# Kernel optimization log

Hardware: AMD Instinct MI355X
Metric: run time of the kernel (lower is better)

Reference implementation:

```python
import jax, jax.numpy as jnp
import numpy as np

MAX_DISP = 40
STRIDE_2 = 1
EPS = 1e-06  # hardcoded in the torch module's CosineSimilarity


def setup_inputs() -> dict:
    key = jax.random.key(0)
    k1, k2 = jax.random.split(key)
    B, C, H, W = 4, 256, 128, 256
    x_1 = jax.random.normal(k1, (B, C, H, W), dtype=jnp.float32)
    x_2 = jax.random.normal(k2, (B, C, H, W), dtype=jnp.float32)
    return {"x_1": x_1, "x_2": x_2}


def reference(x_1, x_2):
    B, C, H, W = x_1.shape
    # pad x_2 on the right of the width axis by max_disp (zeros)
    x2p = jnp.pad(x_2, ((0, 0), (0, 0), (0, 0), (0, MAX_DISP)))
    # channel L2 norms computed ONCE (the fusion opportunity)
    n1 = jnp.sqrt(jnp.sum(x_1 * x_1, axis=1))            # [B, H, W]
    n2p = jnp.sqrt(jnp.sum(x2p * x2p, axis=1))           # [B, H, W+D]
    sims = []
    for d in range(0, MAX_DISP + 1, STRIDE_2):           # fixed small set of 41 shifts
        x2s = jax.lax.dynamic_slice_in_dim(x2p, d, W, axis=3)   # [B, C, H, W]
        n2 = jax.lax.dynamic_slice_in_dim(n2p, d, W, axis=2)    # [B, H, W]
        dot = jnp.einsum('bchw,bchw->bhw', x_1, x2s)
        sims.append(dot / jnp.maximum(n1 * n2, EPS))
    return jnp.stack(sims, axis=1)                       # [B, 41, H, W]
```

## Files before the change

kernel.cpp:

```cpp
#include <hip/hip_runtime.h>
#include <hip/hip_bf16.h>


#define B_   4
#define C_   256
#define H_   128
#define W_   256
#define ND_  41
#define HW_  (H_ * W_)
#define CHW_ (C_ * HW_)
#define EPS_ 1e-6f

typedef __attribute__((ext_vector_type(4))) float f32x4;
typedef __attribute__((ext_vector_type(8))) short bf16x8;

#define ABASE 0
#define BBASE 20480
#define NBASE 44800
#define LDSZ  47040

#define PHASE_BAR() do {                                         \
    __builtin_amdgcn_sched_barrier(0);                           \
    asm volatile("s_waitcnt lgkmcnt(0)" ::: "memory");           \
    __builtin_amdgcn_s_barrier();                                \
    __builtin_amdgcn_sched_barrier(0);                           \
  } while (0)

__device__ __forceinline__ unsigned bfr(float x) {
  unsigned u = __builtin_bit_cast(unsigned, x);
  return (u + 0x7fffu + ((u >> 16) & 1u)) >> 16;
}

__global__ __launch_bounds__(512, 4)
void corr_mfma(const float* __restrict__ x1, const float* __restrict__ x2,
               float* __restrict__ out) {
  __shared__ __align__(16) char lds[LDSZ];

  const int tid = threadIdx.x;
  const int l   = tid & 63;
  const int v   = tid >> 6;
  const int m   = l & 15;
  const int g   = l >> 4;

  const int r = blockIdx.x;
  const int b = r >> 7;
  const int h = r & (H_ - 1);

  const float* X1 = x1 + b * CHW_ + h * W_;
  const float* X2 = x2 + b * CHW_ + h * W_;

  if (tid < 560) ((float*)(lds + NBASE))[tid] = 0.f;
  {
    unsigned* zp = (unsigned*)(lds + BBASE + 256 * 80);
    zp[tid] = 0u;
    if (tid < 960 - 512) zp[tid + 512] = 0u;
  }

  int wadr1[4];
#pragma unroll
  for (int j = 0; j < 4; ++j) {
    int w = 4 * l + j;
    wadr1[j] = ABASE + w * 80 + (((v >> 1) + w) % 5) * 16 + (v & 1) * 8;
  }
  int adrA[2], adrB[2][4];
#pragma unroll
  for (int i = 0; i < 2; ++i) {
    int wt = v + 8 * i;
    int rowA = 16 * wt + m;
    adrA[i] = ABASE + rowA * 80 + ((g + rowA) % 5) * 16;
#pragma unroll
    for (int c = 0; c < 4; ++c) {
      int col = 16 * (wt + c) + m;
      adrB[i][c] = BBASE + col * 80 + ((g + col) % 5) * 16;
    }
  }

  f32x4 acc[2][4];
#pragma unroll
  for (int i = 0; i < 2; ++i)
#pragma unroll
    for (int c = 0; c < 4; ++c) acc[i][c] = (f32x4){0.f, 0.f, 0.f, 0.f};
  float ssq1[4] = {0.f, 0.f, 0.f, 0.f}, ssq2[4] = {0.f, 0.f, 0.f, 0.f};

  f32x4 r1[4], r2[4];
  auto loadset = [&](int ks) {
    const float* p1 = X1 + (ks * 32 + 4 * v) * HW_ + 4 * l;
    const float* p2 = X2 + (ks * 32 + 4 * v) * HW_ + 4 * l;
#pragma unroll
    for (int i = 0; i < 4; ++i) {
      r1[i] = *(const f32x4*)(p1 + i * HW_);
      r2[i] = *(const f32x4*)(p2 + i * HW_);
    }
  };

  loadset(0);

  for (int ks = 0; ks < 8; ++ks) {
    PHASE_BAR();
#pragma unroll
    for (int j = 0; j < 4; ++j) {
#pragma unroll
      for (int i = 0; i < 4; ++i) {
        ssq1[j] += r1[i][j] * r1[i][j];
        ssq2[j] += r2[i][j] * r2[i][j];
      }
      uint2 p1, p2;
      p1.x = bfr(r1[0][j]) | (bfr(r1[1][j]) << 16);
      p1.y = bfr(r1[2][j]) | (bfr(r1[3][j]) << 16);
      p2.x = bfr(r2[0][j]) | (bfr(r2[1][j]) << 16);
      p2.y = bfr(r2[2][j]) | (bfr(r2[3][j]) << 16);
      *(uint2*)(lds + wadr1[j]) = p1;
      *(uint2*)(lds + wadr1[j] + (BBASE - ABASE)) = p2;
    }
    if (ks < 7) loadset(ks + 1);
    PHASE_BAR();
    bf16x8 a0 = *(const bf16x8*)(lds + adrA[0]);
    bf16x8 a1 = *(const bf16x8*)(lds + adrA[1]);
#pragma unroll
    for (int c = 0; c < 4; ++c) {
      bf16x8 b0 = *(const bf16x8*)(lds + adrB[0][c]);
      acc[0][c] = __builtin_amdgcn_mfma_f32_16x16x32_bf16(a0, b0, acc[0][c], 0, 0, 0);
    }
#pragma unroll
    for (int c = 0; c < 4; ++c) {
      bf16x8 b1 = *(const bf16x8*)(lds + adrB[1][c]);
      acc[1][c] = __builtin_amdgcn_mfma_f32_16x16x32_bf16(a1, b1, acc[1][c], 0, 0, 0);
    }
  }

  float* nsq = (float*)(lds + NBASE);
#pragma unroll
  for (int j = 0; j < 4; ++j) {
    atomicAdd(nsq + 4 * l + j, ssq1[j]);
    atomicAdd(nsq + 256 + 4 * l + j, ssq2[j]);
  }
  __syncthreads();
  if (tid < 512) nsq[tid] = sqrtf(nsq[tid]);
  if (tid < 48)  nsq[512 + tid] = sqrtf(nsq[512 + tid]);
  __syncthreads();

  float* Sw  = (float*)(lds + v * 4224);
  float* n1s = nsq;
  float* n2s = nsq + 256;
  const int wq = l & 3, dd = l >> 2;
#pragma unroll
  for (int i = 0; i < 2; ++i) {
    int wt = v + 8 * i;
#pragma unroll
    for (int c = 0; c < 4; ++c)
#pragma unroll
      for (int rr = 0; rr < 4; ++rr)
        Sw[(4 * g + rr) * 66 + 16 * c + m] = acc[i][c][rr];
#pragma unroll
    for (int p = 0; p < 3; ++p) {
      int d  = 16 * p + dd;
      int w0 = 16 * wt + 4 * wq;
      f32x4 o;
#pragma unroll
      for (int j = 0; j < 4; ++j) {
        int mm = 4 * wq + j;
        float dot = Sw[mm * 66 + mm + d];
        o[j] = dot / fmaxf(n1s[w0 + j] * n2s[w0 + j + d], EPS_);
      }
      if (d <= 40)
        *(f32x4*)(out + ((b * ND_ + d) * H_ + h) * W_ + w0) = o;
    }
  }
}

extern "C" void kernel_launch(void* const* d_in, const int* in_sizes, int n_in,
                              void* d_out, int out_size, void* d_ws, size_t ws_size,
                              hipStream_t stream) {
  const float* x1 = (const float*)d_in[0];
  const float* x2 = (const float*)d_in[1];
  float* out = (float*)d_out;
  dim3 grid(B_ * H_);
  dim3 block(512);
  hipLaunchKernelGGL(corr_mfma, grid, block, 0, stream, x1, x2, out);
}
```

Measured before the change: 58.19 us.

## Double-buffer global loads two K-steps ahead with named register sets

Replaces the single register staging set with two alternating sets (A/B) and fully unrolls the eight K-steps, so global loads are issued two iterations ahead instead of one. This aims to hide more HBM latency behind the pack and MFMA phases. It doubles the staging registers (32 extra VGPRs), which may hurt occupancy under the 512x4 launch bound or cause spills.

```diff
diff --git a/kernel.cpp b/kernel.cpp
--- a/kernel.cpp
+++ b/kernel.cpp
@@ -82,51 +82,65 @@
     for (int c = 0; c < 4; ++c) acc[i][c] = (f32x4){0.f, 0.f, 0.f, 0.f};
   float ssq1[4] = {0.f, 0.f, 0.f, 0.f}, ssq2[4] = {0.f, 0.f, 0.f, 0.f};
 
-  f32x4 r1[4], r2[4];
-  auto loadset = [&](int ks) {
-    const float* p1 = X1 + (ks * 32 + 4 * v) * HW_ + 4 * l;
-    const float* p2 = X2 + (ks * 32 + 4 * v) * HW_ + 4 * l;
-#pragma unroll
-    for (int i = 0; i < 4; ++i) {
-      r1[i] = *(const f32x4*)(p1 + i * HW_);
-      r2[i] = *(const f32x4*)(p2 + i * HW_);
-    }
-  };
+  f32x4 r1A0, r1A1, r1A2, r1A3, r2A0, r2A1, r2A2, r2A3;
+  f32x4 r1B0, r1B1, r1B2, r1B3, r2B0, r2B1, r2B2, r2B3;
 
-  loadset(0);
+#define LOADSET(S, ks_) do {                                         \
+    const float* _p1 = X1 + ((ks_) * 32 + 4 * v) * HW_ + 4 * l;      \
+    const float* _p2 = X2 + ((ks_) * 32 + 4 * v) * HW_ + 4 * l;      \
+    r1##S##0 = *(const f32x4*)(_p1);           r2##S##0 = *(const f32x4*)(_p2);           \
+    r1##S##1 = *(const f32x4*)(_p1 + HW_);     r2##S##1 = *(const f32x4*)(_p2 + HW_);     \
+    r1##S##2 = *(const f32x4*)(_p1 + 2 * HW_); r2##S##2 = *(const f32x4*)(_p2 + 2 * HW_); \
+    r1##S##3 = *(const f32x4*)(_p1 + 3 * HW_); r2##S##3 = *(const f32x4*)(_p2 + 3 * HW_); \
+  } while (0)
 
-  for (int ks = 0; ks < 8; ++ks) {
-    PHASE_BAR();
-#pragma unroll
-    for (int j = 0; j < 4; ++j) {
-#pragma unroll
-      for (int i = 0; i < 4; ++i) {
-        ssq1[j] += r1[i][j] * r1[i][j];
-        ssq2[j] += r2[i][j] * r2[i][j];
-      }
-      uint2 p1, p2;
-      p1.x = bfr(r1[0][j]) | (bfr(r1[1][j]) << 16);
-      p1.y = bfr(r1[2][j]) | (bfr(r1[3][j]) << 16);
-      p2.x = bfr(r2[0][j]) | (bfr(r2[1][j]) << 16);
-      p2.y = bfr(r2[2][j]) | (bfr(r2[3][j]) << 16);
-      *(uint2*)(lds + wadr1[j]) = p1;
-      *(uint2*)(lds + wadr1[j] + (BBASE - ABASE)) = p2;
-    }
-    if (ks < 7) loadset(ks + 1);
-    PHASE_BAR();
-    bf16x8 a0 = *(const bf16x8*)(lds + adrA[0]);
-    bf16x8 a1 = *(const bf16x8*)(lds + adrA[1]);
-#pragma unroll
-    for (int c = 0; c < 4; ++c) {
-      bf16x8 b0 = *(const bf16x8*)(lds + adrB[0][c]);
-      acc[0][c] = __builtin_amdgcn_mfma_f32_16x16x32_bf16(a0, b0, acc[0][c], 0, 0, 0);
-    }
-#pragma unroll
-    for (int c = 0; c < 4; ++c) {
-      bf16x8 b1 = *(const bf16x8*)(lds + adrB[1][c]);
-      acc[1][c] = __builtin_amdgcn_mfma_f32_16x16x32_bf16(a1, b1, acc[1][c], 0, 0, 0);
-    }
-  }
+#define PACK(S) do {                                                          \
+    _Pragma("unroll")                                                         \
+    for (int j = 0; j < 4; ++j) {                                             \
+      ssq1[j] += r1##S##0[j] * r1##S##0[j] + r1##S##1[j] * r1##S##1[j]        \
+               + r1##S##2[j] * r1##S##2[j] + r1##S##3[j] * r1##S##3[j];       \
+      ssq2[j] += r2##S##0[j] * r2##S##0[j] + r2##S##1[j] * r2##S##1[j]        \
+               + r2##S##2[j] * r2##S##2[j] + r2##S##3[j] * r2##S##3[j];       \
+      uint2 q1, q2;                                                           \
+      q1.x = bfr(r1##S##0[j]) | (bfr(r1##S##1[j]) << 16);                     \
+      q1.y = bfr(r1##S##2[j]) | (bfr(r1##S##3[j]) << 16);                     \
+      q2.x = bfr(r2##S##0[j]) | (bfr(r2##S##1[j]) << 16);                     \
+      q2.y = bfr(r2##S##2[j]) | (bfr(r2##S##3[j]) << 16);                     \
+      *(uint2*)(lds + wadr1[j]) = q1;                                         \
+      *(uint2*)(lds + wadr1[j] + BBASE) = q2;                                 \
+    }                                                                         \
+  } while (0)
+
+#define MFMA_STEP() do {                                                      \
+    bf16x8 a0 = *(const bf16x8*)(lds + adrA[0]);                              \
+    bf16x8 a1 = *(const bf16x8*)(lds + adrA[1]);                              \
+    _Pragma("unroll")                                                         \
+    for (int c = 0; c < 4; ++c) {                                             \
+      bf16x8 b0 = *(const bf16x8*)(lds + adrB[0][c]);                         \
+      acc[0][c] = __builtin_amdgcn_mfma_f32_16x16x32_bf16(a0, b0, acc[0][c], 0, 0, 0); \
+    }                                                                         \
+    _Pragma("unroll")                                                         \
+    for (int c = 0; c < 4; ++c) {                                             \
+      bf16x8 b1 = *(const bf16x8*)(lds + adrB[1][c]);                         \
+      acc[1][c] = __builtin_amdgcn_mfma_f32_16x16x32_bf16(a1, b1, acc[1][c], 0, 0, 0); \
+    }                                                                         \
+  } while (0)
+
+#define BODY(S, ks_) do {                                                     \
+    PHASE_BAR();                              \
+    PACK(S);                                 \
+    if ((ks_) < 6) LOADSET(S, (ks_) + 2);       \
+    PHASE_BAR();                                          \
+    MFMA_STEP();                                                              \
+  } while (0)
+
+  LOADSET(A, 0);
+  LOADSET(B, 1);
+
+  BODY(A, 0); BODY(B, 1);
+  BODY(A, 2); BODY(B, 3);
+  BODY(A, 4); BODY(B, 5);
+  BODY(A, 6); BODY(B, 7);
 
   float* nsq = (float*)(lds + NBASE);
 #pragma unroll
```

Measured after the change: 97.45 us. +67.5%, slower.

## Split each row across two blocks with an x2 halo for finer-grained work

Applied to the files above, without the earlier changes.

Each block now handles half a row (128 columns) with 256 threads instead of a full row with 512 threads, which doubles the grid. The first half loads an extra 40-column halo of x2; the second half writes zeros for the padding instead. Shared memory per block drops by about half, so more blocks can fit per CU and work spreads more evenly across CUs. The cost is redundant halo reads of x2 and extra per-block setup and norm reduction.

```diff
diff --git a/kernel.cpp b/kernel.cpp
--- a/kernel.cpp
+++ b/kernel.cpp
@@ -15,9 +15,9 @@
 typedef __attribute__((ext_vector_type(8))) short bf16x8;
 
 #define ABASE 0
-#define BBASE 20480
-#define NBASE 44800
-#define LDSZ  47040
+#define BBASE 10240
+#define NBASE 24320
+#define LDSZ  25504
 
 #define PHASE_BAR() do {                                         \
     __builtin_amdgcn_sched_barrier(0);                           \
@@ -31,7 +31,7 @@
   return (u + 0x7fffu + ((u >> 16) & 1u)) >> 16;
 }
 
-__global__ __launch_bounds__(512, 4)
+__global__ __launch_bounds__(256, 4)
 void corr_mfma(const float* __restrict__ x1, const float* __restrict__ x2,
                float* __restrict__ out) {
   __shared__ __align__(16) char lds[LDSZ];
@@ -41,31 +41,33 @@
   const int v   = tid >> 6;
   const int m   = l & 15;
   const int g   = l >> 4;
+  const int q   = l & 31;
+  const int h2  = l >> 5;
 
-  const int r = blockIdx.x;
-  const int b = r >> 7;
-  const int h = r & (H_ - 1);
+  const int r    = blockIdx.x;
+  const int half = r & 1;
+  const int hh   = (r >> 1) & (H_ - 1);
+  const int b    = r >> 8;
+  const int wb   = 128 * half;
 
-  const float* X1 = x1 + b * CHW_ + h * W_;
-  const float* X2 = x2 + b * CHW_ + h * W_;
+  const float* X1 = x1 + b * CHW_ + hh * W_ + wb;
+  const float* X2 = x2 + b * CHW_ + hh * W_ + wb;
 
-  if (tid < 560) ((float*)(lds + NBASE))[tid] = 0.f;
-  {
-    unsigned* zp = (unsigned*)(lds + BBASE + 256 * 80);
-    zp[tid] = 0u;
-    if (tid < 960 - 512) zp[tid + 512] = 0u;
-  }
+  for (int i = tid; i < 296; i += 256) ((float*)(lds + NBASE))[i] = 0.f;
 
-  int wadr1[4];
+  int wadrA[4], wadrBa[4], wadrBb[4];
 #pragma unroll
-  for (int j = 0; j < 4; ++j) {
-    int w = 4 * l + j;
-    wadr1[j] = ABASE + w * 80 + (((v >> 1) + w) % 5) * 16 + (v & 1) * 8;
+  for (int jj = 0; jj < 4; ++jj) {
+    int wa = 4 * q + jj;
+    wadrA[jj]  = ABASE + wa * 80 + ((v + wa) % 5) * 16 + 8 * h2;
+    wadrBa[jj] = BBASE + wa * 80 + ((v + wa) % 5) * 16 + 8 * h2;
+    int wbb = 128 + 4 * q + jj;
+    wadrBb[jj] = BBASE + wbb * 80 + ((v + wbb) % 5) * 16 + 8 * h2;
   }
   int adrA[2], adrB[2][4];
 #pragma unroll
   for (int i = 0; i < 2; ++i) {
-    int wt = v + 8 * i;
+    int wt = v + 4 * i;
     int rowA = 16 * wt + m;
     adrA[i] = ABASE + rowA * 80 + ((g + rowA) % 5) * 16;
 #pragma unroll
@@ -80,16 +82,22 @@
   for (int i = 0; i < 2; ++i)
 #pragma unroll
     for (int c = 0; c < 4; ++c) acc[i][c] = (f32x4){0.f, 0.f, 0.f, 0.f};
-  float ssq1[4] = {0.f, 0.f, 0.f, 0.f}, ssq2[4] = {0.f, 0.f, 0.f, 0.f};
+  float ssq1[4]  = {0.f, 0.f, 0.f, 0.f};
+  float ssq2a[4] = {0.f, 0.f, 0.f, 0.f};
+  float ssq2b[4] = {0.f, 0.f, 0.f, 0.f};
 
-  f32x4 r1[4], r2[4];
+  const bool ldb = (q < 10) && (half == 0);
+
+  f32x4 r1[4], r2a[4], r2b[4];
   auto loadset = [&](int ks) {
-    const float* p1 = X1 + (ks * 32 + 4 * v) * HW_ + 4 * l;
-    const float* p2 = X2 + (ks * 32 + 4 * v) * HW_ + 4 * l;
+    const float* p1 = X1 + (ks * 32 + 8 * v + 4 * h2) * HW_ + 4 * q;
+    const float* p2 = X2 + (ks * 32 + 8 * v + 4 * h2) * HW_ + 4 * q;
 #pragma unroll
-    for (int i = 0; i < 4; ++i) {
-      r1[i] = *(const f32x4*)(p1 + i * HW_);
-      r2[i] = *(const f32x4*)(p2 + i * HW_);
+    for (int j = 0; j < 4; ++j) {
+      r1[j]  = *(const f32x4*)(p1 + j * HW_);
+      r2a[j] = *(const f32x4*)(p2 + j * HW_);
+      r2b[j] = ldb ? *(const f32x4*)(p2 + j * HW_ + 128)
+                   : (f32x4){0.f, 0.f, 0.f, 0.f};
     }
   };
 
@@ -98,19 +106,26 @@
   for (int ks = 0; ks < 8; ++ks) {
     PHASE_BAR();
 #pragma unroll
-    for (int j = 0; j < 4; ++j) {
-#pragma unroll
-      for (int i = 0; i < 4; ++i) {
-        ssq1[j] += r1[i][j] * r1[i][j];
-        ssq2[j] += r2[i][j] * r2[i][j];
+    for (int jj = 0; jj < 4; ++jj) {
+      ssq1[jj]  += r1[0][jj] * r1[0][jj] + r1[1][jj] * r1[1][jj]
+                 + r1[2][jj] * r1[2][jj] + r1[3][jj] * r1[3][jj];
+      ssq2a[jj] += r2a[0][jj] * r2a[0][jj] + r2a[1][jj] * r2a[1][jj]
+                 + r2a[2][jj] * r2a[2][jj] + r2a[3][jj] * r2a[3][jj];
+      ssq2b[jj] += r2b[0][jj] * r2b[0][jj] + r2b[1][jj] * r2b[1][jj]
+                 + r2b[2][jj] * r2b[2][jj] + r2b[3][jj] * r2b[3][jj];
+      uint2 q1, q2;
+      q1.x = bfr(r1[0][jj]) | (bfr(r1[1][jj]) << 16);
+      q1.y = bfr(r1[2][jj]) | (bfr(r1[3][jj]) << 16);
+      q2.x = bfr(r2a[0][jj]) | (bfr(r2a[1][jj]) << 16);
+      q2.y = bfr(r2a[2][jj]) | (bfr(r2a[3][jj]) << 16);
+      *(uint2*)(lds + wadrA[jj])  = q1;
+      *(uint2*)(lds + wadrBa[jj]) = q2;
+      if (q < 10) {
+        uint2 q3;
+        q3.x = bfr(r2b[0][jj]) | (bfr(r2b[1][jj]) << 16);
+        q3.y = bfr(r2b[2][jj]) | (bfr(r2b[3][jj]) << 16);
+        *(uint2*)(lds + wadrBb[jj]) = q3;
       }
-      uint2 p1, p2;
-      p1.x = bfr(r1[0][j]) | (bfr(r1[1][j]) << 16);
-      p1.y = bfr(r1[2][j]) | (bfr(r1[3][j]) << 16);
-      p2.x = bfr(r2[0][j]) | (bfr(r2[1][j]) << 16);
-      p2.y = bfr(r2[2][j]) | (bfr(r2[3][j]) << 16);
-      *(uint2*)(lds + wadr1[j]) = p1;
-      *(uint2*)(lds + wadr1[j] + (BBASE - ABASE)) = p2;
     }
     if (ks < 7) loadset(ks + 1);
     PHASE_BAR();
@@ -130,40 +145,41 @@
 
   float* nsq = (float*)(lds + NBASE);
 #pragma unroll
-  for (int j = 0; j < 4; ++j) {
-    atomicAdd(nsq + 4 * l + j, ssq1[j]);
-    atomicAdd(nsq + 256 + 4 * l + j, ssq2[j]);
+  for (int jj = 0; jj < 4; ++jj) {
+    atomicAdd(nsq + 4 * q + jj, ssq1[jj]);
+    atomicAdd(nsq + 128 + 4 * q + jj, ssq2a[jj]);
+    if (q < 10) atomicAdd(nsq + 256 + 4 * q + jj, ssq2b[jj]);
   }
   __syncthreads();
-  if (tid < 512) nsq[tid] = sqrtf(nsq[tid]);
-  if (tid < 48)  nsq[512 + tid] = sqrtf(nsq[512 + tid]);
+  for (int i = tid; i < 296; i += 256) nsq[i] = sqrtf(nsq[i]);
   __syncthreads();
 
   float* Sw  = (float*)(lds + v * 4224);
   float* n1s = nsq;
-  float* n2s = nsq + 256;
+  float* n2s = nsq + 128;
   const int wq = l & 3, dd = l >> 2;
 #pragma unroll
   for (int i = 0; i < 2; ++i) {
-    int wt = v + 8 * i;
+    int wt = v + 4 * i;
 #pragma unroll
     for (int c = 0; c < 4; ++c)
 #pragma unroll
       for (int rr = 0; rr < 4; ++rr)
         Sw[(4 * g + rr) * 66 + 16 * c + m] = acc[i][c][rr];
+    const int w0 = 16 * wt + 4 * wq;
 #pragma unroll
     for (int p = 0; p < 3; ++p) {
-      int d  = 16 * p + dd;
-      int w0 = 16 * wt + 4 * wq;
-      f32x4 o;
+      int d = 16 * p + dd;
+      if (d <= 40) {
+        f32x4 o;
 #pragma unroll
-      for (int j = 0; j < 4; ++j) {
-        int mm = 4 * wq + j;
-        float dot = Sw[mm * 66 + mm + d];
-        o[j] = dot / fmaxf(n1s[w0 + j] * n2s[w0 + j + d], EPS_);
+        for (int j = 0; j < 4; ++j) {
+          int mm = 4 * wq + j;
+          float dot = Sw[mm * 66 + mm + d];
+          o[j] = dot / fmaxf(n1s[w0 + j] * n2s[w0 + j + d], EPS_);
+        }
+        *(f32x4*)(out + ((b * ND_ + d) * H_ + hh) * W_ + wb + w0) = o;
       }
-      if (d <= 40)
-        *(f32x4*)(out + ((b * ND_ + d) * H_ + h) * W_ + w0) = o;
     }
   }
 }
@@ -174,7 +190,7 @@
   const float* x1 = (const float*)d_in[0];
   const float* x2 = (const float*)d_in[1];
   float* out = (float*)d_out;
-  dim3 grid(B_ * H_);
-  dim3 block(512);
+  dim3 grid(B_ * H_ * 2);
+  dim3 block(256);
   hipLaunchKernelGGL(corr_mfma, grid, block, 0, stream, x1, x2, out);
 }
```

Measured after the change: 170.2 us. 192% more time.
